# Performance work log

Measured on AMD Instinct MI355X. Metric: run time of the kernel, lower is better.

Reference implementation:

```python
import jax, jax.numpy as jnp
import numpy as np

N_NODES = 100000
N_EDGES = 1000000
H = 128  # hidden_size


def setup_inputs() -> dict:
    key = jax.random.key(0)
    ks = jax.random.split(key, 8)
    emb = jax.random.normal(ks[0], (N_NODES, H), dtype=jnp.float32)
    edge_index = jax.random.randint(ks[1], (2, N_EDGES), 0, N_NODES, dtype=jnp.int64)
    # MLP([2H, 4H, H, 1]) weights (Kaiming-ish scaled normals)
    W1 = jax.random.normal(ks[2], (2 * H, 4 * H), dtype=jnp.float32) / np.sqrt(2 * H).astype(np.float32)
    b1 = jnp.zeros((4 * H,), dtype=jnp.float32)
    W2 = jax.random.normal(ks[3], (4 * H, H), dtype=jnp.float32) / np.sqrt(4 * H).astype(np.float32)
    b2 = jnp.zeros((H,), dtype=jnp.float32)
    W3 = jax.random.normal(ks[4], (H, 1), dtype=jnp.float32) / np.sqrt(H).astype(np.float32)
    b3 = jnp.zeros((1,), dtype=jnp.float32)
    return {"emb": emb, "edge_index": edge_index,
            "W1": W1, "b1": b1, "W2": W2, "b2": b2, "W3": W3, "b3": b3}


def reference(emb, edge_index, W1, b1, W2, b2, W3, b3):
    # ExtractorMLP.forward with learn_edge_att=True, eval mode.
    col = edge_index[0]
    row = edge_index[1]
    # edge-gather + concat: [E, 2H]
    f12 = jnp.concatenate([emb[col], emb[row]], axis=-1)
    # MLP([2H, 4H, H, 1]); Dropout is identity in eval mode
    h = jax.nn.relu(f12 @ W1 + b1)          # [E, 4H]
    h = jax.nn.relu(h @ W2 + b2)            # [E, H]
    att_log_logits = h @ W3 + b3            # [E, 1]
    # concrete_sample with training=False -> plain sigmoid
    att = jax.nn.sigmoid(att_log_logits)
    return att
```

## Files before the change

kernel.cpp:

```cpp
#include <hip/hip_runtime.h>
#include <math.h>

#define E_TOTAL   1000000
#define HDIM      128
#define K1        256
#define N1        512
#define N2        128
#define M_TILE    64
#define BLOCK     256

typedef _Float16 f16;
typedef _Float16 f16_4  __attribute__((ext_vector_type(4)));
typedef _Float16 f16_8  __attribute__((ext_vector_type(8)));
typedef float    f32_16 __attribute__((ext_vector_type(16)));

__global__ void prep_weights(const float* __restrict__ W1, const float* __restrict__ W2,
                             f16* __restrict__ W1F, f16* __restrict__ W2F) {
    int t = blockIdx.x * blockDim.x + threadIdx.x;
    const int total1 = K1 * N1;
    const int total2 = N1 * N2;
    if (t < total1) {
        int v    = t & 7;
        int lane = (t >> 3) & 63;
        int kc   = (t >> 9) & 15;
        int nt   = t >> 13;
        int k = kc * 16 + (lane >> 5) * 8 + v;
        int n = nt * 32 + (lane & 31);
        W1F[t] = (f16)W1[k * N1 + n];
    } else if (t < total1 + total2) {
        int u = t - total1;
        int v    = u & 7;
        int lane = (u >> 3) & 63;
        int kcg  = (u >> 9) & 31;
        int nt   = u >> 14;
        int k = kcg * 16 + (lane >> 5) * 8 + v;
        int n = nt * 32 + (lane & 31);
        W2F[u] = (f16)W2[k * N2 + n];
    }
}

__global__ void prep_emb(const float* __restrict__ emb, f16* __restrict__ emb16) {
    int t = blockIdx.x * blockDim.x + threadIdx.x;
    float4 f = ((const float4*)emb)[t];
    f16_4 v = { (f16)f.x, (f16)f.y, (f16)f.z, (f16)f.w };
    ((f16_4*)emb16)[t] = v;
}

template <bool F16EMB>
__global__ __launch_bounds__(BLOCK, 3) void edge_mlp_kernel(
    const float* __restrict__ emb,
    const f16*   __restrict__ emb16,
    const int*   __restrict__ eidx,
    const f16*   __restrict__ W1F,
    const float* __restrict__ b1,
    const f16*   __restrict__ W2F,
    const float* __restrict__ b2,
    const float* __restrict__ W3,
    const float* __restrict__ b3,
    float* __restrict__ out)
{
    __shared__ __align__(16) f16 sAF[2 * 16 * 64 * 8];
    __shared__ __align__(16) f16 sBF[2 * 8 * 64 * 8];
    f16* sH2F = sAF;

    const int tid = threadIdx.x;
    const int e0  = blockIdx.x * M_TILE;

    {
        const int m    = tid >> 2;
        const int side = (tid >> 1) & 1;
        const int sub  = tid & 1;
        const int met  = m >> 5;
        const int m31  = m & 31;
        const int node = eidx[side * E_TOTAL + e0 + m];
        if (F16EMB) {
            const f16* src = emb16 + (size_t)node * HDIM;
            #pragma unroll
            for (int j = 0; j < 4; ++j) {
                const int g = side * 8 + sub * 4 + j;
                const int koff = (sub * 4 + j) * 16;
                #pragma unroll
                for (int lh = 0; lh < 2; ++lh) {
                    f16_8 v = *(const f16_8*)(src + koff + lh * 8);
                    *(f16_8*)(sAF + (((met * 16 + g) * 64 + lh * 32 + m31) << 3)) = v;
                }
            }
        } else {
            const float* src = emb + (size_t)node * HDIM;
            #pragma unroll
            for (int j = 0; j < 4; ++j) {
                const int g = side * 8 + sub * 4 + j;
                const int koff = (sub * 4 + j) * 16;
                #pragma unroll
                for (int lh = 0; lh < 2; ++lh) {
                    float4 fa = *(const float4*)(src + koff + lh * 8);
                    float4 fb = *(const float4*)(src + koff + lh * 8 + 4);
                    f16_8 v = { (f16)fa.x, (f16)fa.y, (f16)fa.z, (f16)fa.w,
                                (f16)fb.x, (f16)fb.y, (f16)fb.z, (f16)fb.w };
                    *(f16_8*)(sAF + (((met * 16 + g) * 64 + lh * 32 + m31) << 3)) = v;
                }
            }
        }
    }
    __syncthreads();

    const int wnt  = tid >> 6;
    const int lane = tid & 63;
    const int l31  = lane & 31;
    const int lh   = lane >> 5;

    f32_16 acc2[2] = {{0.f}, {0.f}};

    {
        f32_16 acc1[2] = {{0.f}, {0.f}};
        const int nt = wnt;
        #pragma unroll
        for (int kc = 0; kc < 16; ++kc) {
            f16_8 wf = *(const f16_8*)(W1F + (((nt * 16 + kc) * 64 + lane) << 3));
            #pragma unroll
            for (int et = 0; et < 2; ++et) {
                f16_8 ef = *(const f16_8*)(sAF + (((et * 16 + kc) * 64 + lane) << 3));
                acc1[et] = __builtin_amdgcn_mfma_f32_32x32x16_f16(wf, ef, acc1[et], 0, 0, 0);
            }
        }
        #pragma unroll
        for (int et = 0; et < 2; ++et) {
            #pragma unroll
            for (int g = 0; g < 4; ++g) {
                const int wnl = wnt * 32 + lh * 4 + g * 8;
                const float4 bv = *(const float4*)(b1 + wnl);
                f16_4 hv;
                #pragma unroll
                for (int i = 0; i < 4; ++i) {
                    float v = acc1[et][g * 4 + i] + ((const float*)&bv)[i];
                    hv[i] = (f16)(v > 0.f ? v : 0.f);
                }
                const int kl = wnt * 2 + (g >> 1);
                *(f16_4*)(sBF + ((((et * 8 + kl) * 64 + (g & 1) * 32 + l31) << 3) + lh * 4)) = hv;
            }
        }
    }
    __syncthreads();

    #pragma unroll
    for (int q = 1; q < 4; ++q) {
        f32_16 acc1[2] = {{0.f}, {0.f}};
        const int nt = q * 4 + wnt;
        #pragma unroll
        for (int kc = 0; kc < 16; ++kc) {
            f16_8 wf = *(const f16_8*)(W1F + (((nt * 16 + kc) * 64 + lane) << 3));
            #pragma unroll
            for (int et = 0; et < 2; ++et) {
                f16_8 ef = *(const f16_8*)(sAF + (((et * 16 + kc) * 64 + lane) << 3));
                acc1[et] = __builtin_amdgcn_mfma_f32_32x32x16_f16(wf, ef, acc1[et], 0, 0, 0);
            }
            if (kc < 8) {
                const int kcg = (q - 1) * 8 + kc;
                f16_8 wf2 = *(const f16_8*)(W2F + (((wnt * 32 + kcg) * 64 + lane) << 3));
                #pragma unroll
                for (int et = 0; et < 2; ++et) {
                    f16_8 ef2 = *(const f16_8*)(sBF + (((et * 8 + kc) * 64 + lane) << 3));
                    acc2[et] = __builtin_amdgcn_mfma_f32_32x32x16_f16(wf2, ef2, acc2[et], 0, 0, 0);
                }
            }
        }
        __syncthreads();
        #pragma unroll
        for (int et = 0; et < 2; ++et) {
            #pragma unroll
            for (int g = 0; g < 4; ++g) {
                const int wnl = wnt * 32 + lh * 4 + g * 8;
                const float4 bv = *(const float4*)(b1 + q * 128 + wnl);
                f16_4 hv;
                #pragma unroll
                for (int i = 0; i < 4; ++i) {
                    float v = acc1[et][g * 4 + i] + ((const float*)&bv)[i];
                    hv[i] = (f16)(v > 0.f ? v : 0.f);
                }
                const int kl = wnt * 2 + (g >> 1);
                *(f16_4*)(sBF + ((((et * 8 + kl) * 64 + (g & 1) * 32 + l31) << 3) + lh * 4)) = hv;
            }
        }
        __syncthreads();
    }

    {
        #pragma unroll
        for (int kc = 0; kc < 8; ++kc) {
            const int kcg = 24 + kc;
            f16_8 wf2 = *(const f16_8*)(W2F + (((wnt * 32 + kcg) * 64 + lane) << 3));
            #pragma unroll
            for (int et = 0; et < 2; ++et) {
                f16_8 ef2 = *(const f16_8*)(sBF + (((et * 8 + kc) * 64 + lane) << 3));
                acc2[et] = __builtin_amdgcn_mfma_f32_32x32x16_f16(wf2, ef2, acc2[et], 0, 0, 0);
            }
        }
    }

    {
        #pragma unroll
        for (int et = 0; et < 2; ++et) {
            #pragma unroll
            for (int g = 0; g < 4; ++g) {
                const int wn = wnt * 32 + lh * 4 + g * 8;
                const float4 bv = *(const float4*)(b2 + wn);
                f16_4 hv;
                #pragma unroll
                for (int i = 0; i < 4; ++i) {
                    float v = acc2[et][g * 4 + i] + ((const float*)&bv)[i];
                    hv[i] = (f16)(v > 0.f ? v : 0.f);
                }
                const int kl = wnt * 2 + (g >> 1);
                *(f16_4*)(sH2F + ((((et * 8 + kl) * 64 + (g & 1) * 32 + l31) << 3) + lh * 4)) = hv;
            }
        }
    }
    __syncthreads();

    {
        const int m   = tid >> 2;
        const int j   = tid & 3;
        const int met = m >> 5;
        const int m31 = m & 31;
        float s = 0.f;
        #pragma unroll
        for (int jj = 0; jj < 2; ++jj) {
            const int kl = j * 2 + jj;
            f16_8 a = *(const f16_8*)(sH2F + (((met * 8 + kl) * 64 + m31) << 3));
            f16_8 b = *(const f16_8*)(sH2F + (((met * 8 + kl) * 64 + 32 + m31) << 3));
            const float4* w3v = (const float4*)(W3 + kl * 16);
            float4 w0 = w3v[0], w1 = w3v[1], w2 = w3v[2], w3q = w3v[3];
            s += (float)a[0]*w0.x + (float)a[1]*w0.y + (float)a[2]*w0.z + (float)a[3]*w0.w;
            s += (float)a[4]*w1.x + (float)a[5]*w1.y + (float)a[6]*w1.z + (float)a[7]*w1.w;
            s += (float)b[0]*w2.x + (float)b[1]*w2.y + (float)b[2]*w2.z + (float)b[3]*w2.w;
            s += (float)b[4]*w3q.x + (float)b[5]*w3q.y + (float)b[6]*w3q.z + (float)b[7]*w3q.w;
        }
        s += __shfl_xor(s, 1);
        s += __shfl_xor(s, 2);
        if (j == 0) {
            const float logit = s + b3[0];
            out[e0 + m] = 1.0f / (1.0f + __expf(-logit));
        }
    }
}

extern "C" void kernel_launch(void* const* d_in, const int* in_sizes, int n_in,
                              void* d_out, int out_size, void* d_ws, size_t ws_size,
                              hipStream_t stream) {
    const float* emb  = (const float*)d_in[0];
    const int*   eidx = (const int*)d_in[1];
    const float* W1   = (const float*)d_in[2];
    const float* b1   = (const float*)d_in[3];
    const float* W2   = (const float*)d_in[4];
    const float* b2   = (const float*)d_in[5];
    const float* W3   = (const float*)d_in[6];
    const float* b3   = (const float*)d_in[7];
    float* out = (float*)d_out;

    const size_t wbytes   = (size_t)(K1 * N1 + N1 * N2) * sizeof(f16);
    const size_t embbytes = (size_t)100000 * HDIM * sizeof(f16);

    f16* W1F = (f16*)d_ws;
    f16* W2F = W1F + K1 * N1;

    const int prep_total = K1 * N1 + N1 * N2;
    prep_weights<<<(prep_total + 255) / 256, 256, 0, stream>>>(W1, W2, W1F, W2F);

    if (ws_size >= wbytes + embbytes) {
        f16* emb16 = W2F + N1 * N2;
        const int cvt_threads = 100000 * HDIM / 4;
        prep_emb<<<cvt_threads / 256, 256, 0, stream>>>(emb, emb16);
        edge_mlp_kernel<true><<<E_TOTAL / M_TILE, BLOCK, 0, stream>>>(
            emb, emb16, eidx, W1F, b1, W2F, b2, W3, b3, out);
    } else {
        edge_mlp_kernel<false><<<E_TOTAL / M_TILE, BLOCK, 0, stream>>>(
            emb, (const f16*)nullptr, eidx, W1F, b1, W2F, b2, W3, b3, out);
    }
}
```

Measured before the change: 562.6 us.

## Make edge MLP kernel persistent and prefetch next tile's embeddings via global_load_lds

Measured after the change: 1.136 ms. +101.8%, slower.

```diff
diff --git a/kernel.cpp b/kernel.cpp
--- a/kernel.cpp
+++ b/kernel.cpp
@@ -8,11 +8,17 @@
 #define N2        128
 #define M_TILE    64
 #define BLOCK     256
+#define GRID_P    1536
 
 typedef _Float16 f16;
 typedef _Float16 f16_4  __attribute__((ext_vector_type(4)));
 typedef _Float16 f16_8  __attribute__((ext_vector_type(8)));
 typedef float    f32_16 __attribute__((ext_vector_type(16)));
+typedef unsigned int u32;
+
+#define GLD_LDS16(srcp, dstp) __builtin_amdgcn_global_load_lds( \
+    (const __attribute__((address_space(1))) u32*)(const void*)(srcp), \
+    (__attribute__((address_space(3))) u32*)(void*)(dstp), 16, 0, 0)
 
 __global__ void prep_weights(const float* __restrict__ W1, const float* __restrict__ W2,
                              f16* __restrict__ W1F, f16* __restrict__ W2F) {
@@ -61,101 +67,156 @@
 {
     __shared__ __align__(16) f16 sAF[2 * 16 * 64 * 8];
     __shared__ __align__(16) f16 sBF[2 * 8 * 64 * 8];
-    f16* sH2F = sAF;
-
-    const int tid = threadIdx.x;
-    const int e0  = blockIdx.x * M_TILE;
-
-    {
-        const int m    = tid >> 2;
-        const int side = (tid >> 1) & 1;
-        const int sub  = tid & 1;
-        const int met  = m >> 5;
-        const int m31  = m & 31;
-        const int node = eidx[side * E_TOTAL + e0 + m];
-        if (F16EMB) {
-            const f16* src = emb16 + (size_t)node * HDIM;
-            #pragma unroll
-            for (int j = 0; j < 4; ++j) {
-                const int g = side * 8 + sub * 4 + j;
-                const int koff = (sub * 4 + j) * 16;
-                #pragma unroll
-                for (int lh = 0; lh < 2; ++lh) {
-                    f16_8 v = *(const f16_8*)(src + koff + lh * 8);
-                    *(f16_8*)(sAF + (((met * 16 + g) * 64 + lh * 32 + m31) << 3)) = v;
-                }
-            }
-        } else {
-            const float* src = emb + (size_t)node * HDIM;
-            #pragma unroll
-            for (int j = 0; j < 4; ++j) {
-                const int g = side * 8 + sub * 4 + j;
-                const int koff = (sub * 4 + j) * 16;
-                #pragma unroll
-                for (int lh = 0; lh < 2; ++lh) {
-                    float4 fa = *(const float4*)(src + koff + lh * 8);
-                    float4 fb = *(const float4*)(src + koff + lh * 8 + 4);
-                    f16_8 v = { (f16)fa.x, (f16)fa.y, (f16)fa.z, (f16)fa.w,
-                                (f16)fb.x, (f16)fb.y, (f16)fb.z, (f16)fb.w };
-                    *(f16_8*)(sAF + (((met * 16 + g) * 64 + lh * 32 + m31) << 3)) = v;
-                }
-            }
-        }
-    }
-    __syncthreads();
-
+    f16* sH2F = sBF;
+
+    const int tid  = threadIdx.x;
     const int wnt  = tid >> 6;
     const int lane = tid & 63;
     const int l31  = lane & 31;
     const int lh   = lane >> 5;
-
-    f32_16 acc2[2] = {{0.f}, {0.f}};
-
-    {
-        f32_16 acc1[2] = {{0.f}, {0.f}};
-        const int nt = wnt;
+    const int met  = wnt >> 1;
+    const int side = wnt & 1;
+    const int NT   = E_TOTAL / M_TILE;
+
+    if (F16EMB) {
+        const int nd = eidx[side * E_TOTAL + blockIdx.x * M_TILE + met * 32 + l31];
+        const f16* nrow = emb16 + (size_t)nd * HDIM;
         #pragma unroll
-        for (int kc = 0; kc < 16; ++kc) {
-            f16_8 wf = *(const f16_8*)(W1F + (((nt * 16 + kc) * 64 + lane) << 3));
+        for (int s = 0; s < 8; ++s)
+            GLD_LDS16(nrow + s * 16 + lh * 8, sAF + (wnt * 8 + s) * 512);
+    }
+
+    for (int tile = blockIdx.x; tile < NT; tile += GRID_P) {
+        const int e0 = tile * M_TILE;
+
+        if (F16EMB) {
+            asm volatile("s_waitcnt vmcnt(0)" ::: "memory");
+            __builtin_amdgcn_s_barrier();
+            __builtin_amdgcn_sched_barrier(0);
+        } else {
+            __syncthreads();
+            const int m    = tid >> 2;
+            const int sd   = (tid >> 1) & 1;
+            const int sub  = tid & 1;
+            const int mt   = m >> 5;
+            const int m31  = m & 31;
+            const int node = eidx[sd * E_TOTAL + e0 + m];
+            const float* src = emb + (size_t)node * HDIM;
+            #pragma unroll
+            for (int j = 0; j < 4; ++j) {
+                const int g    = sd * 8 + sub * 4 + j;
+                const int koff = (sub * 4 + j) * 16;
+                #pragma unroll
+                for (int q2 = 0; q2 < 2; ++q2) {
+                    float4 fa = *(const float4*)(src + koff + q2 * 8);
+                    float4 fb = *(const float4*)(src + koff + q2 * 8 + 4);
+                    f16_8 v = { (f16)fa.x, (f16)fa.y, (f16)fa.z, (f16)fa.w,
+                                (f16)fb.x, (f16)fb.y, (f16)fb.z, (f16)fb.w };
+                    *(f16_8*)(sAF + (((mt * 16 + g) * 64 + q2 * 32 + m31) << 3)) = v;
+                }
+            }
+            __syncthreads();
+        }
+
+        const int tnext = tile + GRID_P;
+        int ndn = 0;
+        if (F16EMB && tnext < NT)
+            ndn = eidx[side * E_TOTAL + tnext * M_TILE + met * 32 + l31];
+
+        f32_16 acc2[2] = {{0.f}, {0.f}};
+
+        {
+            f32_16 acc1[2] = {{0.f}, {0.f}};
+            const int nt = wnt;
+            #pragma unroll
+            for (int kc = 0; kc < 16; ++kc) {
+                f16_8 wf = *(const f16_8*)(W1F + (((nt * 16 + kc) * 64 + lane) << 3));
+                #pragma unroll
+                for (int et = 0; et < 2; ++et) {
+                    f16_8 ef = *(const f16_8*)(sAF + (((et * 16 + kc) * 64 + lane) << 3));
+                    acc1[et] = __builtin_amdgcn_mfma_f32_32x32x16_f16(wf, ef, acc1[et], 0, 0, 0);
+                }
+            }
             #pragma unroll
             for (int et = 0; et < 2; ++et) {
-                f16_8 ef = *(const f16_8*)(sAF + (((et * 16 + kc) * 64 + lane) << 3));
-                acc1[et] = __builtin_amdgcn_mfma_f32_32x32x16_f16(wf, ef, acc1[et], 0, 0, 0);
-            }
-        }
+                #pragma unroll
+                for (int g = 0; g < 4; ++g) {
+                    const int wnl = wnt * 32 + lh * 4 + g * 8;
+                    const float4 bv = *(const float4*)(b1 + wnl);
+                    f16_4 hv;
+                    #pragma unroll
+                    for (int i = 0; i < 4; ++i) {
+                        float v = acc1[et][g * 4 + i] + ((const float*)&bv)[i];
+                        hv[i] = (f16)(v > 0.f ? v : 0.f);
+                    }
+                    const int kl = wnt * 2 + (g >> 1);
+                    *(f16_4*)(sBF + ((((et * 8 + kl) * 64 + (g & 1) * 32 + l31) << 3) + lh * 4)) = hv;
+                }
+            }
+        }
+        __syncthreads();
+
         #pragma unroll
-        for (int et = 0; et < 2; ++et) {
-            #pragma unroll
-            for (int g = 0; g < 4; ++g) {
-                const int wnl = wnt * 32 + lh * 4 + g * 8;
-                const float4 bv = *(const float4*)(b1 + wnl);
-                f16_4 hv;
-                #pragma unroll
-                for (int i = 0; i < 4; ++i) {
-                    float v = acc1[et][g * 4 + i] + ((const float*)&bv)[i];
-                    hv[i] = (f16)(v > 0.f ? v : 0.f);
-                }
-                const int kl = wnt * 2 + (g >> 1);
-                *(f16_4*)(sBF + ((((et * 8 + kl) * 64 + (g & 1) * 32 + l31) << 3) + lh * 4)) = hv;
-            }
-        }
-    }
-    __syncthreads();
-
-    #pragma unroll
-    for (int q = 1; q < 4; ++q) {
-        f32_16 acc1[2] = {{0.f}, {0.f}};
-        const int nt = q * 4 + wnt;
-        #pragma unroll
-        for (int kc = 0; kc < 16; ++kc) {
-            f16_8 wf = *(const f16_8*)(W1F + (((nt * 16 + kc) * 64 + lane) << 3));
+        for (int q = 1; q < 4; ++q) {
+            f32_16 acc1[2] = {{0.f}, {0.f}};
+            const int nt = q * 4 + wnt;
+            #pragma unroll
+            for (int kc = 0; kc < 16; ++kc) {
+                f16_8 wf = *(const f16_8*)(W1F + (((nt * 16 + kc) * 64 + lane) << 3));
+                #pragma unroll
+                for (int et = 0; et < 2; ++et) {
+                    f16_8 ef = *(const f16_8*)(sAF + (((et * 16 + kc) * 64 + lane) << 3));
+                    acc1[et] = __builtin_amdgcn_mfma_f32_32x32x16_f16(wf, ef, acc1[et], 0, 0, 0);
+                }
+                if (kc < 8) {
+                    const int kcg = (q - 1) * 8 + kc;
+                    f16_8 wf2 = *(const f16_8*)(W2F + (((wnt * 32 + kcg) * 64 + lane) << 3));
+                    #pragma unroll
+                    for (int et = 0; et < 2; ++et) {
+                        f16_8 ef2 = *(const f16_8*)(sBF + (((et * 8 + kc) * 64 + lane) << 3));
+                        acc2[et] = __builtin_amdgcn_mfma_f32_32x32x16_f16(wf2, ef2, acc2[et], 0, 0, 0);
+                    }
+                }
+            }
+            __syncthreads();
+
+            if (q == 3 && F16EMB && tnext < NT) {
+                __builtin_amdgcn_sched_barrier(0);
+                const f16* nrow = emb16 + (size_t)ndn * HDIM;
+                #pragma unroll
+                for (int s = 0; s < 8; ++s)
+                    GLD_LDS16(nrow + s * 16 + lh * 8, sAF + (wnt * 8 + s) * 512);
+            }
+
             #pragma unroll
             for (int et = 0; et < 2; ++et) {
-                f16_8 ef = *(const f16_8*)(sAF + (((et * 16 + kc) * 64 + lane) << 3));
-                acc1[et] = __builtin_amdgcn_mfma_f32_32x32x16_f16(wf, ef, acc1[et], 0, 0, 0);
-            }
-            if (kc < 8) {
-                const int kcg = (q - 1) * 8 + kc;
+                #pragma unroll
+                for (int g = 0; g < 4; ++g) {
+                    const int wnl = wnt * 32 + lh * 4 + g * 8;
+                    const float4 bv = *(const float4*)(b1 + q * 128 + wnl);
+                    f16_4 hv;
+                    #pragma unroll
+                    for (int i = 0; i < 4; ++i) {
+                        float v = acc1[et][g * 4 + i] + ((const float*)&bv)[i];
+                        hv[i] = (f16)(v > 0.f ? v : 0.f);
+                    }
+                    const int kl = wnt * 2 + (g >> 1);
+                    *(f16_4*)(sBF + ((((et * 8 + kl) * 64 + (g & 1) * 32 + l31) << 3) + lh * 4)) = hv;
+                }
+            }
+            if (q < 3) {
+                __syncthreads();
+            } else {
+                asm volatile("s_waitcnt lgkmcnt(0)" ::: "memory");
+                __builtin_amdgcn_s_barrier();
+                __builtin_amdgcn_sched_barrier(0);
+            }
+        }
+
+        {
+            #pragma unroll
+            for (int kc = 0; kc < 8; ++kc) {
+                const int kcg = 24 + kc;
                 f16_8 wf2 = *(const f16_8*)(W2F + (((wnt * 32 + kcg) * 64 + lane) << 3));
                 #pragma unroll
                 for (int et = 0; et < 2; ++et) {
@@ -164,82 +225,55 @@
                 }
             }
         }
-        __syncthreads();
-        #pragma unroll
-        for (int et = 0; et < 2; ++et) {
-            #pragma unroll
-            for (int g = 0; g < 4; ++g) {
-                const int wnl = wnt * 32 + lh * 4 + g * 8;
-                const float4 bv = *(const float4*)(b1 + q * 128 + wnl);
-                f16_4 hv;
-                #pragma unroll
-                for (int i = 0; i < 4; ++i) {
-                    float v = acc1[et][g * 4 + i] + ((const float*)&bv)[i];
-                    hv[i] = (f16)(v > 0.f ? v : 0.f);
-                }
-                const int kl = wnt * 2 + (g >> 1);
-                *(f16_4*)(sBF + ((((et * 8 + kl) * 64 + (g & 1) * 32 + l31) << 3) + lh * 4)) = hv;
-            }
-        }
-        __syncthreads();
-    }
-
-    {
-        #pragma unroll
-        for (int kc = 0; kc < 8; ++kc) {
-            const int kcg = 24 + kc;
-            f16_8 wf2 = *(const f16_8*)(W2F + (((wnt * 32 + kcg) * 64 + lane) << 3));
+        __builtin_amdgcn_s_barrier();
+        __builtin_amdgcn_sched_barrier(0);
+
+        {
             #pragma unroll
             for (int et = 0; et < 2; ++et) {
-                f16_8 ef2 = *(const f16_8*)(sBF + (((et * 8 + kc) * 64 + lane) << 3));
-                acc2[et] = __builtin_amdgcn_mfma_f32_32x32x16_f16(wf2, ef2, acc2[et], 0, 0, 0);
-            }
-        }
-    }
-
-    {
-        #pragma unroll
-        for (int et = 0; et < 2; ++et) {
-            #pragma unroll
-            for (int g = 0; g < 4; ++g) {
-                const int wn = wnt * 32 + lh * 4 + g * 8;
-                const float4 bv = *(const float4*)(b2 + wn);
-                f16_4 hv;
-                #pragma unroll
-                for (int i = 0; i < 4; ++i) {
-                    float v = acc2[et][g * 4 + i] + ((const float*)&bv)[i];
-                    hv[i] = (f16)(v > 0.f ? v : 0.f);
-                }
-                const int kl = wnt * 2 + (g >> 1);
-                *(f16_4*)(sH2F + ((((et * 8 + kl) * 64 + (g & 1) * 32 + l31) << 3) + lh * 4)) = hv;
-            }
-        }
-    }
-    __syncthreads();
-
-    {
-        const int m   = tid >> 2;
-        const int j   = tid & 3;
-        const int met = m >> 5;
-        const int m31 = m & 31;
-        float s = 0.f;
-        #pragma unroll
-        for (int jj = 0; jj < 2; ++jj) {
-            const int kl = j * 2 + jj;
-            f16_8 a = *(const f16_8*)(sH2F + (((met * 8 + kl) * 64 + m31) << 3));
-            f16_8 b = *(const f16_8*)(sH2F + (((met * 8 + kl) * 64 + 32 + m31) << 3));
-            const float4* w3v = (const float4*)(W3 + kl * 16);
-            float4 w0 = w3v[0], w1 = w3v[1], w2 = w3v[2], w3q = w3v[3];
-            s += (float)a[0]*w0.x + (float)a[1]*w0.y + (float)a[2]*w0.z + (float)a[3]*w0.w;
-            s += (float)a[4]*w1.x + (float)a[5]*w1.y + (float)a[6]*w1.z + (float)a[7]*w1.w;
-            s += (float)b[0]*w2.x + (float)b[1]*w2.y + (float)b[2]*w2.z + (float)b[3]*w2.w;
-            s += (float)b[4]*w3q.x + (float)b[5]*w3q.y + (float)b[6]*w3q.z + (float)b[7]*w3q.w;
-        }
-        s += __shfl_xor(s, 1);
-        s += __shfl_xor(s, 2);
-        if (j == 0) {
-            const float logit = s + b3[0];
-            out[e0 + m] = 1.0f / (1.0f + __expf(-logit));
+                #pragma unroll
+                for (int g = 0; g < 4; ++g) {
+                    const int wn = wnt * 32 + lh * 4 + g * 8;
+                    const float4 bv = *(const float4*)(b2 + wn);
+                    f16_4 hv;
+                    #pragma unroll
+                    for (int i = 0; i < 4; ++i) {
+                        float v = acc2[et][g * 4 + i] + ((const float*)&bv)[i];
+                        hv[i] = (f16)(v > 0.f ? v : 0.f);
+                    }
+                    const int kl = wnt * 2 + (g >> 1);
+                    *(f16_4*)(sH2F + ((((et * 8 + kl) * 64 + (g & 1) * 32 + l31) << 3) + lh * 4)) = hv;
+                }
+            }
+        }
+        asm volatile("s_waitcnt lgkmcnt(0)" ::: "memory");
+        __builtin_amdgcn_s_barrier();
+        __builtin_amdgcn_sched_barrier(0);
+
+        {
+            const int m   = tid >> 2;
+            const int j   = tid & 3;
+            const int mt  = m >> 5;
+            const int m31 = m & 31;
+            float s = 0.f;
+            #pragma unroll
+            for (int jj = 0; jj < 2; ++jj) {
+                const int kl = j * 2 + jj;
+                f16_8 a = *(const f16_8*)(sH2F + (((mt * 8 + kl) * 64 + m31) << 3));
+                f16_8 b = *(const f16_8*)(sH2F + (((mt * 8 + kl) * 64 + 32 + m31) << 3));
+                const float4* w3v = (const float4*)(W3 + kl * 16);
+                float4 w0 = w3v[0], w1 = w3v[1], w2 = w3v[2], w3q = w3v[3];
+                s += (float)a[0]*w0.x + (float)a[1]*w0.y + (float)a[2]*w0.z + (float)a[3]*w0.w;
+                s += (float)a[4]*w1.x + (float)a[5]*w1.y + (float)a[6]*w1.z + (float)a[7]*w1.w;
+                s += (float)b[0]*w2.x + (float)b[1]*w2.y + (float)b[2]*w2.z + (float)b[3]*w2.w;
+                s += (float)b[4]*w3q.x + (float)b[5]*w3q.y + (float)b[6]*w3q.z + (float)b[7]*w3q.w;
+            }
+            s += __shfl_xor(s, 1);
+            s += __shfl_xor(s, 2);
+            if (j == 0) {
+                const float logit = s + b3[0];
+                out[e0 + m] = 1.0f / (1.0f + __expf(-logit));
+            }
         }
     }
 }
@@ -270,10 +304,10 @@
         f16* emb16 = W2F + N1 * N2;
         const int cvt_threads = 100000 * HDIM / 4;
         prep_emb<<<cvt_threads / 256, 256, 0, stream>>>(emb, emb16);
-        edge_mlp_kernel<true><<<E_TOTAL / M_TILE, BLOCK, 0, stream>>>(
+        edge_mlp_kernel<true><<<GRID_P, BLOCK, 0, stream>>>(
             emb, emb16, eidx, W1F, b1, W2F, b2, W3, b3, out);
     } else {
-        edge_mlp_kernel<false><<<E_TOTAL / M_TILE, BLOCK, 0, stream>>>(
+        edge_mlp_kernel<false><<<GRID_P, BLOCK, 0, stream>>>(
             emb, (const f16*)nullptr, eidx, W1F, b1, W2F, b2, W3, b3, out);
     }
 }
```

## Precompute per-node first-layer projections and gather them per edge

Applied to the files above, without the earlier changes.

Result: slower. 759.5 us (+35.0%).

```diff
diff --git a/kernel.cpp b/kernel.cpp
--- a/kernel.cpp
+++ b/kernel.cpp
@@ -2,6 +2,7 @@
 #include <math.h>
 
 #define E_TOTAL   1000000
+#define N_NODES   100000
 #define HDIM      128
 #define K1        256
 #define N1        512
@@ -46,6 +47,206 @@
     ((f16_4*)emb16)[t] = v;
 }
 
+__global__ __launch_bounds__(BLOCK, 2) void precompute_AB(
+    const float* __restrict__ emb, const f16* __restrict__ W1F,
+    const float* __restrict__ b1,
+    f16* __restrict__ Atab, f16* __restrict__ Btab)
+{
+    __shared__ __align__(16) f16 sNF[2 * 8 * 64 * 8];
+    __shared__ __align__(16) f16 sOut[2 * 64 * 132];
+
+    const int tid = threadIdx.x;
+    const int n0  = blockIdx.x * 64;
+
+    {
+        const int nn = tid >> 2;
+        const int c  = tid & 3;
+        int gn = n0 + nn; if (gn >= N_NODES) gn = N_NODES - 1;
+        const float* src = emb + (size_t)gn * HDIM + c * 32;
+        const int et  = nn >> 5;
+        const int m31 = nn & 31;
+        #pragma unroll
+        for (int u = 0; u < 4; ++u) {
+            float4 fa = *(const float4*)(src + u * 8);
+            float4 fb = *(const float4*)(src + u * 8 + 4);
+            f16_8 v = { (f16)fa.x, (f16)fa.y, (f16)fa.z, (f16)fa.w,
+                        (f16)fb.x, (f16)fb.y, (f16)fb.z, (f16)fb.w };
+            const int kc  = c * 2 + (u >> 1);
+            const int lh2 = u & 1;
+            *(f16_8*)(sNF + (((et * 8 + kc) * 64 + ((lh2 * 32 + m31) ^ kc)) << 3)) = v;
+        }
+    }
+    __syncthreads();
+
+    const int w    = tid >> 6;
+    const int lane = tid & 63;
+    const int l31  = lane & 31;
+    const int lh   = lane >> 5;
+
+    #pragma unroll
+    for (int q = 0; q < 4; ++q) {
+        #pragma unroll
+        for (int T = 0; T < 2; ++T) {
+            f32_16 acc[2] = {{0.f}, {0.f}};
+            #pragma unroll
+            for (int kc = 0; kc < 8; ++kc) {
+                f16_8 wf = *(const f16_8*)(W1F +
+                    ((((q * 4 + w) * 16 + T * 8 + kc) * 64 + lane) << 3));
+                #pragma unroll
+                for (int et = 0; et < 2; ++et) {
+                    f16_8 nf = *(const f16_8*)(sNF +
+                        (((et * 8 + kc) * 64 + (lane ^ kc)) << 3));
+                    acc[et] = __builtin_amdgcn_mfma_f32_32x32x16_f16(wf, nf, acc[et], 0, 0, 0);
+                }
+            }
+            #pragma unroll
+            for (int et = 0; et < 2; ++et) {
+                #pragma unroll
+                for (int g = 0; g < 4; ++g) {
+                    f16_4 hv;
+                    #pragma unroll
+                    for (int i = 0; i < 4; ++i) {
+                        float v = acc[et][g * 4 + i];
+                        if (T == 0) v += b1[q * 128 + w * 32 + g * 8 + lh * 4 + i];
+                        hv[i] = (f16)v;
+                    }
+                    *(f16_4*)(&sOut[(T * 64 + et * 32 + l31) * 132 + w * 32 + g * 8 + lh * 4]) = hv;
+                }
+            }
+        }
+        __syncthreads();
+        {
+            const int nn = tid >> 2;
+            const int c  = tid & 3;
+            const int gn = n0 + nn;
+            if (gn < N_NODES) {
+                #pragma unroll
+                for (int T = 0; T < 2; ++T) {
+                    f16* dst = (T ? Btab : Atab) + (size_t)gn * 512 + q * 128 + c * 32;
+                    #pragma unroll
+                    for (int u = 0; u < 4; ++u)
+                        *(f16_8*)(dst + u * 8) =
+                            *(const f16_8*)(&sOut[(T * 64 + nn) * 132 + c * 32 + u * 8]);
+                }
+            }
+        }
+        __syncthreads();
+    }
+}
+
+__global__ __launch_bounds__(BLOCK, 4) void edge_mlp2(
+    const f16* __restrict__ Atab, const f16* __restrict__ Btab,
+    const int* __restrict__ eidx,
+    const f16* __restrict__ W2F, const float* __restrict__ b2,
+    const float* __restrict__ W3, const float* __restrict__ b3,
+    float* __restrict__ out)
+{
+    __shared__ __align__(16) f16 sHF[2 * 16 * 64 * 8];
+    f16* sH2F = sHF;
+
+    const int tid = threadIdx.x;
+    const int e0  = blockIdx.x * M_TILE;
+
+    const int m    = tid >> 2;
+    const int side = (tid >> 1) & 1;
+    const int sub  = tid & 1;
+    const int met  = m >> 5;
+    const int m31  = m & 31;
+    const int col  = eidx[e0 + m];
+    const int row  = eidx[E_TOTAL + e0 + m];
+    const f16* arow = Atab + (size_t)col * 512;
+    const f16* brow = Btab + (size_t)row * 512;
+
+    const int w    = tid >> 6;
+    const int lane = tid & 63;
+    const int l31  = lane & 31;
+    const int lh   = lane >> 5;
+
+    f32_16 acc2[2] = {{0.f}, {0.f}};
+
+    #pragma unroll
+    for (int h = 0; h < 2; ++h) {
+        #pragma unroll
+        for (int j = 0; j < 4; ++j) {
+            const int g   = side * 8 + sub * 4 + j;
+            const int nof = h * 256 + g * 16;
+            const int psi = side * 4 + sub * 2 + (j & 1);
+            #pragma unroll
+            for (int lh2 = 0; lh2 < 2; ++lh2) {
+                f16_8 av = *(const f16_8*)(arow + nof + lh2 * 8);
+                f16_8 bv = *(const f16_8*)(brow + nof + lh2 * 8);
+                f16_8 hv;
+                #pragma unroll
+                for (int i = 0; i < 8; ++i) {
+                    float v = (float)av[i] + (float)bv[i];
+                    hv[i] = (f16)(v > 0.f ? v : 0.f);
+                }
+                *(f16_8*)(sHF + (((met * 16 + g) * 64 + ((lh2 * 32 + m31) ^ psi)) << 3)) = hv;
+            }
+        }
+        __syncthreads();
+
+        #pragma unroll
+        for (int kc = 0; kc < 16; ++kc) {
+            const int kcg = h * 16 + kc;
+            const int psi = ((kc >> 3) & 1) * 4 + ((kc >> 2) & 1) * 2 + (kc & 1);
+            f16_8 wf2 = *(const f16_8*)(W2F + (((w * 32 + kcg) * 64 + lane) << 3));
+            #pragma unroll
+            for (int et = 0; et < 2; ++et) {
+                f16_8 ef2 = *(const f16_8*)(sHF + (((et * 16 + kc) * 64 + (lane ^ psi)) << 3));
+                acc2[et] = __builtin_amdgcn_mfma_f32_32x32x16_f16(wf2, ef2, acc2[et], 0, 0, 0);
+            }
+        }
+        __syncthreads();
+    }
+
+    {
+        #pragma unroll
+        for (int et = 0; et < 2; ++et) {
+            #pragma unroll
+            for (int g = 0; g < 4; ++g) {
+                const int wn = w * 32 + lh * 4 + g * 8;
+                const float4 bv = *(const float4*)(b2 + wn);
+                f16_4 hv;
+                #pragma unroll
+                for (int i = 0; i < 4; ++i) {
+                    float v = acc2[et][g * 4 + i] + ((const float*)&bv)[i];
+                    hv[i] = (f16)(v > 0.f ? v : 0.f);
+                }
+                const int kl = w * 2 + (g >> 1);
+                *(f16_4*)(sH2F + ((((et * 8 + kl) * 64 + (g & 1) * 32 + l31) << 3) + lh * 4)) = hv;
+            }
+        }
+    }
+    __syncthreads();
+
+    {
+        const int mm  = tid >> 2;
+        const int j   = tid & 3;
+        const int mt  = mm >> 5;
+        const int mm31 = mm & 31;
+        float s = 0.f;
+        #pragma unroll
+        for (int jj = 0; jj < 2; ++jj) {
+            const int kl = j * 2 + jj;
+            f16_8 a = *(const f16_8*)(sH2F + (((mt * 8 + kl) * 64 + mm31) << 3));
+            f16_8 b = *(const f16_8*)(sH2F + (((mt * 8 + kl) * 64 + 32 + mm31) << 3));
+            const float4* w3v = (const float4*)(W3 + kl * 16);
+            float4 w0 = w3v[0], w1 = w3v[1], w2 = w3v[2], w3q = w3v[3];
+            s += (float)a[0]*w0.x + (float)a[1]*w0.y + (float)a[2]*w0.z + (float)a[3]*w0.w;
+            s += (float)a[4]*w1.x + (float)a[5]*w1.y + (float)a[6]*w1.z + (float)a[7]*w1.w;
+            s += (float)b[0]*w2.x + (float)b[1]*w2.y + (float)b[2]*w2.z + (float)b[3]*w2.w;
+            s += (float)b[4]*w3q.x + (float)b[5]*w3q.y + (float)b[6]*w3q.z + (float)b[7]*w3q.w;
+        }
+        s += __shfl_xor(s, 1);
+        s += __shfl_xor(s, 2);
+        if (j == 0) {
+            const float logit = s + b3[0];
+            out[e0 + m] = 1.0f / (1.0f + __expf(-logit));
+        }
+    }
+}
+
 template <bool F16EMB>
 __global__ __launch_bounds__(BLOCK, 3) void edge_mlp_kernel(
     const float* __restrict__ emb,
@@ -65,7 +266,6 @@
 
     const int tid = threadIdx.x;
     const int e0  = blockIdx.x * M_TILE;
-
     {
         const int m    = tid >> 2;
         const int side = (tid >> 1) & 1;
@@ -110,7 +310,6 @@
     const int lh   = lane >> 5;
 
     f32_16 acc2[2] = {{0.f}, {0.f}};
-
     {
         f32_16 acc1[2] = {{0.f}, {0.f}};
         const int nt = wnt;
@@ -183,7 +382,6 @@
         }
         __syncthreads();
     }
-
     {
         #pragma unroll
         for (int kc = 0; kc < 8; ++kc) {
@@ -196,7 +394,6 @@
             }
         }
     }
-
     {
         #pragma unroll
         for (int et = 0; et < 2; ++et) {
@@ -216,7 +413,6 @@
         }
     }
     __syncthreads();
-
     {
         const int m   = tid >> 2;
         const int j   = tid & 3;
@@ -258,7 +454,9 @@
     float* out = (float*)d_out;
 
     const size_t wbytes   = (size_t)(K1 * N1 + N1 * N2) * sizeof(f16);
-    const size_t embbytes = (size_t)100000 * HDIM * sizeof(f16);
+    const size_t embbytes = (size_t)N_NODES * HDIM * sizeof(f16);
+    const size_t tabbytes = (size_t)N_NODES * 512 * sizeof(f16);
+    const size_t need_new = wbytes + 2 * tabbytes;
 
     f16* W1F = (f16*)d_ws;
     f16* W2F = W1F + K1 * N1;
@@ -266,9 +464,15 @@
     const int prep_total = K1 * N1 + N1 * N2;
     prep_weights<<<(prep_total + 255) / 256, 256, 0, stream>>>(W1, W2, W1F, W2F);
 
-    if (ws_size >= wbytes + embbytes) {
+    if (ws_size >= need_new) {
+        f16* Atab = W2F + N1 * N2;
+        f16* Btab = Atab + (size_t)N_NODES * 512;
+        precompute_AB<<<(N_NODES + 63) / 64, BLOCK, 0, stream>>>(emb, W1F, b1, Atab, Btab);
+        edge_mlp2<<<E_TOTAL / M_TILE, BLOCK, 0, stream>>>(
+            Atab, Btab, eidx, W2F, b2, W3, b3, out);
+    } else if (ws_size >= wbytes + embbytes) {
         f16* emb16 = W2F + N1 * N2;
-        const int cvt_threads = 100000 * HDIM / 4;
+        const int cvt_threads = N_NODES * HDIM / 4;
         prep_emb<<<cvt_threads / 256, 256, 0, stream>>>(emb, emb16);
         edge_mlp_kernel<true><<<E_TOTAL / M_TILE, BLOCK, 0, stream>>>(
             emb, emb16, eidx, W1F, b1, W2F, b2, W3, b3, out);
```
